# Kernel optimization log

Hardware: AMD Instinct MI355X
Metric: run time of the kernel (lower is better)

## Reference

```python
import jax, jax.numpy as jnp
import numpy as np
import math

N_CELLS = 65536
HIDDEN = 128
IN_DIM = 64
MAX_DEG = 6
BOND_P = 0.5


def _build_graph():
    """2D lattice bond percolation -> padded adjacency [n, MAX_DEG] + signs + mask."""
    rng = np.random.default_rng(0)
    side = int(math.ceil(math.sqrt(N_CELLS)))
    adj = [[] for _ in range(N_CELLS)]
    for i in range(N_CELLS):
        col = i % side
        r = i + 1
        if col + 1 < side and r < N_CELLS and rng.random() < BOND_P:
            adj[i].append(r); adj[r].append(i)
        d = i + side
        if d < N_CELLS and rng.random() < BOND_P:
            adj[i].append(d); adj[d].append(i)
    for i in range(N_CELLS):  # ring fix for isolated nodes
        if not adj[i]:
            r = (i + 1) % N_CELLS
            adj[i].append(r); adj[r].append(i)
    sign_map = {}
    for i in range(N_CELLS):
        for j in adj[i]:
            key = (min(i, j), max(i, j))
            if key not in sign_map:
                sign_map[key] = 1.0 if rng.random() > 0.5 else -1.0
    nbr = np.zeros((N_CELLS, MAX_DEG), np.int32)
    sgn = np.ones((N_CELLS, MAX_DEG), np.float32)
    msk = np.zeros((N_CELLS, MAX_DEG), bool)
    for i in range(N_CELLS):
        for k, j in enumerate(adj[i][:MAX_DEG]):
            nbr[i, k] = j
            msk[i, k] = True
            sgn[i, k] = sign_map[(min(i, j), max(i, j))]
    return nbr, sgn, msk


def setup_inputs() -> dict:
    key = jax.random.key(0)
    ks = jax.random.split(key, 8)
    nbr, sgn, msk = _build_graph()
    n = N_CELLS
    cell_amp = jax.random.uniform(ks[0], (n, HIDDEN)) * 0.5 + 0.5
    cell_phase = jax.random.normal(ks[1], (n, HIDDEN)) * 0.5 \
        + (2.0 * jnp.pi * jnp.arange(n, dtype=jnp.float32) / n)[:, None]
    phase_vel = jax.random.normal(ks[2], (n, HIDDEN)) * 0.05
    return {
        'x': jax.random.normal(ks[3], (1, IN_DIM)),
        'cell_amp': cell_amp.astype(jnp.float32),
        'cell_phase': cell_phase.astype(jnp.float32),
        'phase_vel': phase_vel.astype(jnp.float32),
        'nbr_idx': jnp.asarray(nbr),
        'nbr_sign': jnp.asarray(sgn),
        'nbr_mask': jnp.asarray(msk),
        'W_in': jax.random.normal(ks[4], (HIDDEN, IN_DIM)) * 0.05,
        'b_in': jax.random.normal(ks[5], (HIDDEN,)) * 0.05,
        'W_dec': jax.random.normal(ks[6], (IN_DIM, 2 * HIDDEN)) * 0.05,
        'b_dec': jax.random.normal(ks[7], (IN_DIM,)) * 0.05,
        'step': 1,
    }


def reference(x, cell_amp, cell_phase, phase_vel, nbr_idx, nbr_sign, nbr_mask,
              W_in, b_in, W_dec, b_dec, step):
    n, h = cell_amp.shape
    # complex cell states, then phase-velocity rotation
    states = (cell_amp * jnp.exp(1j * cell_phase)).astype(jnp.complex64)
    states = states * jnp.exp(1j * phase_vel * 0.1)
    ang = jnp.angle(states)                               # [n, h]

    # --- neighbor interference (vectorized gather over padded adjacency) ---
    nbr_states = states[nbr_idx]                          # [n, d, h]
    nbr_ang = ang[nbr_idx]                                # [n, d, h]
    coupling = jnp.cos(ang[:, None, :] - nbr_ang) * nbr_sign[:, :, None]
    contrib = jnp.where(nbr_mask[:, :, None], coupling * nbr_states * 0.1, 0.0)
    interference = contrib.sum(axis=1)                    # [n, h]
    deg = nbr_mask.sum(axis=-1)                           # [n]
    new = 0.7 * states + 0.3 * interference / jnp.maximum(deg, 1)[:, None]
    new = jnp.where((deg > 0)[:, None], new, states)      # 'continue' for isolated nodes

    # --- morphism toward strongest neighbor (argmax over neighbors) ---
    strength = jnp.abs(states).sum(axis=-1)               # [n]
    nstr = jnp.where(nbr_mask, strength[nbr_idx], -jnp.inf)
    best_slot = jnp.argmax(nstr, axis=1)                  # first max, like python max()
    best = jnp.take_along_axis(nbr_idx, best_slot[:, None], axis=1)[:, 0]
    src = states[best]                                    # [n, h]
    morph = jnp.abs(src) * jnp.exp(1j * (jnp.angle(new) - jnp.angle(src)))
    new = jnp.where((deg >= 2)[:, None], new + 0.02 * morph, new)

    # --- global traveling wave ---
    t = step * 0.1
    wave = 0.02 * jnp.sin(t + 2.0 * jnp.pi * jnp.arange(n, dtype=jnp.float32) / n)
    new = new * (1.0 + wave)[:, None]

    # --- input-driven phase perturbation on first 32 cells ---
    sig = x[0] @ W_in.T + b_in                            # [h]
    pp = sig / (jnp.abs(sig).max() + 1e-8) * jnp.pi * 0.1
    idx = jnp.arange(n, dtype=jnp.float32)
    factor = jnp.where(jnp.arange(n) < 32, 0.1 / (1.0 + 0.1 * idx), 0.0)
    new_ang = jnp.angle(new) + pp[None, :] * factor[:, None]
    new = jnp.abs(new) * jnp.exp(1j * new_ang)

    # --- amplitude renormalization per cell ---
    amp = jnp.abs(new)
    amp = amp / (amp.max(axis=-1, keepdims=True) + 1e-8)
    cs = (amp * jnp.exp(1j * jnp.angle(new))).astype(jnp.complex64)

    # --- readout ---
    mean_state = cs.mean(axis=0)                          # [h]
    out_real = jnp.concatenate([mean_state.real, mean_state.imag])[None, :]
    pred = out_real @ W_dec.T + b_dec                     # [1, IN_DIM]
    tension = jnp.var(jnp.abs(cs), ddof=1)                # torch.var (unbiased)
    return pred, tension
```

## Files before the change

### kernel.cpp

```cpp
#include <hip/hip_runtime.h>
#include <hip/hip_fp16.h>
#include <math.h>

#define N_CELLS 65536
#define HIDDEN  128
#define IN_DIM  64
#define MAX_DEG 6

#define WPB    4
#define NPB    32
#define NBLK   (N_CELLS/NPB)
#define CHUNK  4
#define NXCD   8

#define INV2PI 0.15915494309189535f

typedef _Float16 h2f __attribute__((ext_vector_type(2)));

__device__ __forceinline__ void fsincos(float x, float& s, float& c) {
    const float r = x * INV2PI;
    s = __builtin_amdgcn_sinf(r);
    c = __builtin_amdgcn_cosf(r);
}

#define WS_PP    0
#define WS_FLAG  512
#define WS_STR   1024
#define WS_S     (1024 + N_CELLS*4)
#define WS_ADJ   (WS_S + (size_t)N_CELLS*512)
#define WS_P     (WS_ADJ + (size_t)N_CELLS*32)
#define WS_SA    (WS_P + 256*NBLK*4)
#define WS_SA2   (WS_SA + NBLK*4)
#define WS_MEAN  (WS_SA2 + NBLK*4)

__global__ __launch_bounds__(256) void k_pre(
    const float* __restrict__ amp, const float* __restrict__ phase,
    const float* __restrict__ vel,
    const float* __restrict__ x, const float* __restrict__ W_in,
    const float* __restrict__ b_in, const unsigned char* __restrict__ maskb,
    int4* __restrict__ S, float* __restrict__ strength,
    float* __restrict__ pp, int* __restrict__ flag)
{
    const int tid = threadIdx.x;
    const int bx  = blockIdx.x;
    if (bx < N_CELLS/8) {
        const int blkp = (bx & (NXCD-1)) * (N_CELLS/8/NXCD) + (bx >> 3);
        const int node = blkp*8 + (tid >> 5);
        const int hl   = tid & 31;
        const size_t ro = (size_t)node*HIDDEN + 4*hl;
        const float4 a = *(const float4*)(amp   + ro);
        const float4 p = *(const float4*)(phase + ro);
        const float4 v = *(const float4*)(vel   + ro);
        float s0,c0,s1,c1,s2,c2,s3,c3;
        fsincos(fmaf(0.1f, v.x, p.x), s0, c0);
        fsincos(fmaf(0.1f, v.y, p.y), s1, c1);
        fsincos(fmaf(0.1f, v.z, p.z), s2, c2);
        fsincos(fmaf(0.1f, v.w, p.w), s3, c3);
        union { int4 v4; __half2 h[4]; } u;
        u.h[0] = __floats2half2_rn(a.x*c0, a.x*s0);
        u.h[1] = __floats2half2_rn(a.y*c1, a.y*s1);
        u.h[2] = __floats2half2_rn(a.z*c2, a.z*s2);
        u.h[3] = __floats2half2_rn(a.w*c3, a.w*s3);
        S[(size_t)node*32 + hl] = u.v4;
        float st = a.x + a.y + a.z + a.w;
        #pragma unroll
        for (int off = 16; off > 0; off >>= 1) st += __shfl_xor(st, off);
        if (hl == 0) strength[node] = st;
        return;
    }
    __shared__ float sig[HIDDEN];
    __shared__ float red[HIDDEN];
    __shared__ int fl[256];
    if (tid < HIDDEN) {
        float acc = b_in[tid];
        #pragma unroll 8
        for (int d = 0; d < IN_DIM; ++d) acc = fmaf(W_in[tid*IN_DIM + d], x[d], acc);
        sig[tid] = acc;
        red[tid] = fabsf(acc);
    }
    int v = 0;
    #pragma unroll
    for (int r = 0; r < 4; ++r) v |= (int)maskb[(tid + 256*r)*4 + 1];
    fl[tid] = v;
    __syncthreads();
    for (int s = 64; s > 0; s >>= 1) {
        if (tid < s) red[tid] = fmaxf(red[tid], red[tid + s]);
        __syncthreads();
    }
    for (int s = 128; s > 0; s >>= 1) {
        if (tid < s) fl[tid] |= fl[tid + s];
        __syncthreads();
    }
    if (tid < HIDDEN) pp[tid] = sig[tid] / (red[0] + 1e-8f) * 0.314159265358979f;
    if (tid == 0) *flag = (fl[0] != 0) ? 1 : 0;
}

__global__ __launch_bounds__(256) void k_adj(
    const int* __restrict__ nbr_idx, const float* __restrict__ nbr_sign,
    const void* __restrict__ nbr_mask, const int* __restrict__ flagp,
    const float* __restrict__ strength, int4* __restrict__ adj)
{
    __shared__ int   lw[256][MAX_DEG];
    __shared__ float ls[256][MAX_DEG];
    const int t = threadIdx.x;
    const int bx = blockIdx.x;
    const int blkp = (bx & (NXCD-1)) * (N_CELLS/256/NXCD) + (bx >> 3);
    const int i = blkp*256 + t;
    const int flagv = *flagp;
    const unsigned char* mb = (const unsigned char*)nbr_mask;
    const int*           mi = (const int*)nbr_mask;
    int cnt = 0;
    #pragma unroll
    for (int k = 0; k < MAX_DEG; ++k) {
        const int e = i*MAX_DEG + k;
        const int m = flagv ? (mb[e] != 0) : (mi[e] != 0);
        const int j = nbr_idx[e];
        const float sg = nbr_sign[e];
        if (m) {
            lw[t][cnt] = j | ((sg < 0.0f) ? (1<<24) : 0) | (1<<25);
            ls[t][cnt] = strength[j];
            ++cnt;
        }
    }
    #pragma unroll
    for (int k = 0; k < MAX_DEG; ++k) if (k >= cnt) lw[t][k] = 0;
    int cb = 0; float bv = ls[t][0];
    #pragma unroll
    for (int k = 1; k < MAX_DEG; ++k)
        if (k < cnt && ls[t][k] > bv) { bv = ls[t][k]; cb = k; }
    adj[2*(size_t)i    ] = make_int4(lw[t][0], lw[t][1], lw[t][2], lw[t][3]);
    adj[2*(size_t)i + 1] = make_int4(lw[t][4], lw[t][5], cnt | (cb << 8), 0);
}

__global__ __launch_bounds__(256) void k_mainc(
    const int4* __restrict__ S, const int4* __restrict__ adj,
    const int* __restrict__ step, const float* __restrict__ pp,
    float* __restrict__ P, float* __restrict__ p_sa, float* __restrict__ p_sa2)
{
    __shared__ float4 lredre[WPB][32], lredim[WPB][32];
    __shared__ float  lsa[WPB], lsa2[WPB];

    const int tid   = threadIdx.x;
    const int bx    = blockIdx.x;
    const int blk   = (bx & (NXCD-1)) * (NBLK/NXCD) + (bx >> 3);
    const int node0 = blk * NPB;

    const int wv   = tid >> 6;
    const int lane = tid & 63;
    const int half = lane >> 5;
    const int lh   = lane & 31;
    const float trev = 0.1f * (float)step[0] * INV2PI;
    const float4 ppv = ((const float4*)pp)[lh];

    float accre[4] = {0,0,0,0}, accim[4] = {0,0,0,0};
    float accsa = 0.f, accsa2 = 0.f;

    const int nlbase = wv*(2*CHUNK) + half;
    int4 A0n = adj[2*(size_t)(node0 + nlbase)    ];
    int4 A1n = adj[2*(size_t)(node0 + nlbase) + 1];

    #pragma unroll 1
    for (int c = 0; c < CHUNK; ++c) {
        const int nl = nlbase + 2*c;
        const int i  = node0 + nl;
        const int4 A0 = A0n, A1 = A1n;
        if (c + 1 < CHUNK) {
            A0n = adj[2*(size_t)(i + 2)    ];
            A1n = adj[2*(size_t)(i + 2) + 1];
        }
        const int deg = A1.z & 0xFF;
        const int cb  = A1.z >> 8;
        const int slots[MAX_DEG] = {A0.x, A0.y, A0.z, A0.w, A1.x, A1.y};

        union H { int4 v4; h2f h[4]; int w[4]; };
        H us, nb[MAX_DEG];
        us.v4 = S[(size_t)(unsigned)i*32 + lh];
        #pragma unroll
        for (int k = 0; k < MAX_DEG; ++k)
            if (k < deg) nb[k].v4 = S[(size_t)(unsigned)(slots[k] & 0xFFFF)*32 + lh];

        float R[4], I[4], inva[4];
        #pragma unroll
        for (int q = 0; q < 4; ++q) {
            R[q] = (float)us.h[q].x;
            I[q] = (float)us.h[q].y;
            inva[q] = __builtin_amdgcn_rsqf(
                __builtin_amdgcn_fdot2(us.h[q], us.h[q], 0.0f, false));
        }

        float ir[4] = {0,0,0,0}, ii[4] = {0,0,0,0};
        #pragma unroll
        for (int k = 0; k < MAX_DEG; ++k) {
            if (k < deg) {
                const int w = slots[k];
                const float sgnm = (w & (1<<24)) ? -1.0f : 1.0f;
                #pragma unroll
                for (int q = 0; q < 4; ++q) {
                    const float E   = __builtin_amdgcn_fdot2(us.h[q], nb[k].h[q], 0.0f, false);
                    const float aj2 = __builtin_amdgcn_fdot2(nb[k].h[q], nb[k].h[q], 0.0f, false);
                    const float g = sgnm * E * __builtin_amdgcn_rsqf(aj2);
                    ir[q] = fmaf(g, (float)nb[k].h[q].x, ir[q]);
                    ii[q] = fmaf(g, (float)nb[k].h[q].y, ii[q]);
                }
            }
        }

        H ub;
        #pragma unroll
        for (int q = 0; q < 4; ++q) {
            int v = nb[0].w[q];
            #pragma unroll
            for (int k = 1; k < MAX_DEG; ++k)
                if (k < deg) v = (k == cb) ? nb[k].w[q] : v;
            ub.w[q] = v;
        }

        const float f = 0.03f * __builtin_amdgcn_rcpf((float)deg);
        float nr[4], ni[4];
        #pragma unroll
        for (int q = 0; q < 4; ++q) {
            const float fq = f * inva[q];
            nr[q] = fmaf(0.7f, R[q], fq*ir[q]);
            ni[q] = fmaf(0.7f, I[q], fq*ii[q]);
        }

        if (deg >= 2) {
            #pragma unroll
            for (int q = 0; q < 4; ++q) {
                const float ex = (float)ub.h[q].x, ey = (float)ub.h[q].y;
                const float im = 0.02f * __builtin_amdgcn_rsqf(nr[q]*nr[q] + ni[q]*ni[q]);
                const float mr = im*(nr[q]*ex + ni[q]*ey);
                const float mi = im*(ni[q]*ex - nr[q]*ey);
                nr[q] += mr; ni[q] += mi;
            }
        }

        const float wr = fmaf((float)i, 1.52587890625e-5f, trev);
        const float wf = 1.0f + 0.02f * __builtin_amdgcn_sinf(wr);
        #pragma unroll
        for (int q = 0; q < 4; ++q) { nr[q] *= wf; ni[q] *= wf; }

        if (i < 32) {
            const float fac = 0.1f / fmaf(0.1f, (float)i, 1.0f);
            const float pv[4] = {ppv.x, ppv.y, ppv.z, ppv.w};
            #pragma unroll
            for (int q = 0; q < 4; ++q) {
                float sp, cp;
                fsincos(pv[q]*fac, sp, cp);
                const float tr = nr[q]*cp - ni[q]*sp;
                ni[q] = ni[q]*cp + nr[q]*sp;
                nr[q] = tr;
            }
        }

        float m[4];
        #pragma unroll
        for (int q = 0; q < 4; ++q) m[q] = sqrtf(nr[q]*nr[q] + ni[q]*ni[q]);
        float lm = fmaxf(fmaxf(m[0], m[1]), fmaxf(m[2], m[3]));
        #pragma unroll
        for (int off = 16; off > 0; off >>= 1) lm = fmaxf(lm, __shfl_xor(lm, off));
        const float sc = 1.0f / (lm + 1e-8f);
        #pragma unroll
        for (int q = 0; q < 4; ++q) {
            accre[q] += nr[q]*sc;
            accim[q] += ni[q]*sc;
            const float A = m[q]*sc;
            accsa  += A;
            accsa2 += A*A;
        }
    }

    #pragma unroll
    for (int q = 0; q < 4; ++q) {
        accre[q] += __shfl_xor(accre[q], 32);
        accim[q] += __shfl_xor(accim[q], 32);
    }
    #pragma unroll
    for (int off = 32; off > 0; off >>= 1) {
        accsa  += __shfl_xor(accsa,  off);
        accsa2 += __shfl_xor(accsa2, off);
    }
    if (half == 0) {
        lredre[wv][lh] = make_float4(accre[0], accre[1], accre[2], accre[3]);
        lredim[wv][lh] = make_float4(accim[0], accim[1], accim[2], accim[3]);
    }
    if (lane == 0) { lsa[wv] = accsa; lsa2[wv] = accsa2; }
    __syncthreads();
    if (tid < 32) {
        float4 r = lredre[0][tid], im = lredim[0][tid];
        #pragma unroll
        for (int w = 1; w < WPB; ++w) {
            const float4 a = lredre[w][tid], b = lredim[w][tid];
            r.x += a.x; r.y += a.y; r.z += a.z; r.w += a.w;
            im.x += b.x; im.y += b.y; im.z += b.z; im.w += b.w;
        }
        P[(4*tid  )*NBLK + blk]       = r.x;
        P[(4*tid+1)*NBLK + blk]       = r.y;
        P[(4*tid+2)*NBLK + blk]       = r.z;
        P[(4*tid+3)*NBLK + blk]       = r.w;
        P[(128+4*tid  )*NBLK + blk]   = im.x;
        P[(128+4*tid+1)*NBLK + blk]   = im.y;
        P[(128+4*tid+2)*NBLK + blk]   = im.z;
        P[(128+4*tid+3)*NBLK + blk]   = im.w;
    }
    if (tid == 0) {
        p_sa [blk] = lsa[0]  + lsa[1]  + lsa[2]  + lsa[3];
        p_sa2[blk] = lsa2[0] + lsa2[1] + lsa2[2] + lsa2[3];
    }
}

__global__ void k_red(const float* __restrict__ P, float* __restrict__ mean)
{
    __shared__ double red[256];
    const int r = blockIdx.x, tid = threadIdx.x;
    double s = 0.0;
    #pragma unroll
    for (int k = 0; k < NBLK/256; ++k) s += (double)P[(size_t)r*NBLK + tid + 256*k];
    red[tid] = s;
    __syncthreads();
    for (int st = 128; st > 0; st >>= 1) { if (tid < st) red[tid] += red[tid + st]; __syncthreads(); }
    if (tid == 0) mean[r] = (float)(red[0] / (double)N_CELLS);
}

__global__ void k_final(const float* __restrict__ mean_in,
                        const float* __restrict__ p_sa, const float* __restrict__ p_sa2,
                        const float* __restrict__ W_dec, const float* __restrict__ b_dec,
                        float* __restrict__ out)
{
    __shared__ float  mean[2*HIDDEN];
    __shared__ double dred[256];
    __shared__ double tots[2];
    const int tid = threadIdx.x;
    mean[tid] = mean_in[tid];
    double sa = 0.0, sa2 = 0.0;
    #pragma unroll
    for (int k = 0; k < NBLK/256; ++k) {
        sa  += (double)p_sa [tid + 256*k];
        sa2 += (double)p_sa2[tid + 256*k];
    }
    dred[tid] = sa;
    __syncthreads();
    for (int s = 128; s > 0; s >>= 1) { if (tid < s) dred[tid] += dred[tid + s]; __syncthreads(); }
    if (tid == 0) tots[0] = dred[0];
    __syncthreads();
    dred[tid] = sa2;
    __syncthreads();
    for (int s = 128; s > 0; s >>= 1) { if (tid < s) dred[tid] += dred[tid + s]; __syncthreads(); }
    if (tid == 0) tots[1] = dred[0];
    __syncthreads();

    if (tid < IN_DIM) {
        float acc = b_dec[tid];
        #pragma unroll 8
        for (int c = 0; c < 2*HIDDEN; ++c) acc = fmaf(mean[c], W_dec[tid*2*HIDDEN + c], acc);
        out[tid] = acc;
    }
    if (tid == 0) {
        const double M = (double)N_CELLS * (double)HIDDEN;
        const double var = (tots[1] - tots[0]*tots[0]/M) / (M - 1.0);
        out[IN_DIM] = (float)var;
    }
}

extern "C" void kernel_launch(void* const* d_in, const int* in_sizes, int n_in,
                              void* d_out, int out_size, void* d_ws, size_t ws_size,
                              hipStream_t stream)
{
    const float* x       = (const float*)d_in[0];
    const float* amp     = (const float*)d_in[1];
    const float* phase   = (const float*)d_in[2];
    const float* vel     = (const float*)d_in[3];
    const int*   nbr_idx = (const int*)d_in[4];
    const float* nbr_sgn = (const float*)d_in[5];
    const void*  nbr_msk = d_in[6];
    const float* W_in    = (const float*)d_in[7];
    const float* b_in    = (const float*)d_in[8];
    const float* W_dec   = (const float*)d_in[9];
    const float* b_dec   = (const float*)d_in[10];
    const int*   step    = (const int*)d_in[11];

    char* wsb = (char*)d_ws;
    float* pp    = (float*)(wsb + WS_PP);
    int*   flag  = (int*)  (wsb + WS_FLAG);
    float* strg  = (float*)(wsb + WS_STR);
    int4*  S     = (int4*) (wsb + WS_S);
    int4*  adjv  = (int4*) (wsb + WS_ADJ);
    float* P     = (float*)(wsb + WS_P);
    float* p_sa  = (float*)(wsb + WS_SA);
    float* p_sa2 = (float*)(wsb + WS_SA2);
    float* meanb = (float*)(wsb + WS_MEAN);
    float* out   = (float*)d_out;

    k_pre<<<N_CELLS/8 + 1, 256, 0, stream>>>(amp, phase, vel, x, W_in, b_in,
                                             (const unsigned char*)nbr_msk,
                                             S, strg, pp, flag);
    k_adj<<<N_CELLS/256, 256, 0, stream>>>(nbr_idx, nbr_sgn, nbr_msk, flag, strg, adjv);
    k_mainc<<<NBLK, 256, 0, stream>>>(S, adjv, step, pp, P, p_sa, p_sa2);
    k_red<<<256, 256, 0, stream>>>(P, meanb);
    k_final<<<1, 256, 0, stream>>>(meanb, p_sa, p_sa2, W_dec, b_dec, out);
}
```

Before: 67.27 us.

## Precompute best neighbor in slot 0 and make per-wave gather loop uniform

The adjacency build kernel now swaps the strongest-coupled neighbor into slot 0 and pads empty slots with the node itself. It also stores the max degree of each node pair, and the two half-waves of a wave process such a pair. The main kernel loops to that wave-uniform bound, using a validity bit to zero the padded contributions. This drops the per-lane divergent branches, the cb select over the neighbors, and the divergent deg>=2 branch. The cost is extra gathers of padded self entries, plus a shared-memory sync in the adjacency kernel.

```diff
diff --git a/kernel.cpp b/kernel.cpp
--- a/kernel.cpp
+++ b/kernel.cpp
@@ -102,6 +102,7 @@
 {
     __shared__ int   lw[256][MAX_DEG];
     __shared__ float ls[256][MAX_DEG];
+    __shared__ int   ldeg[256];
     const int t = threadIdx.x;
     const int bx = blockIdx.x;
     const int blkp = (bx & (NXCD-1)) * (N_CELLS/256/NXCD) + (bx >> 3);
@@ -122,14 +123,22 @@
             ++cnt;
         }
     }
-    #pragma unroll
-    for (int k = 0; k < MAX_DEG; ++k) if (k >= cnt) lw[t][k] = 0;
     int cb = 0; float bv = ls[t][0];
     #pragma unroll
     for (int k = 1; k < MAX_DEG; ++k)
         if (k < cnt && ls[t][k] > bv) { bv = ls[t][k]; cb = k; }
+    if (cb != 0) {
+        const int tmp = lw[t][0];
+        lw[t][0] = lw[t][cb];
+        lw[t][cb] = tmp;
+    }
+    #pragma unroll
+    for (int k = 0; k < MAX_DEG; ++k) if (k >= cnt) lw[t][k] = i;
+    ldeg[t] = cnt;
+    __syncthreads();
+    const int kmax = max(cnt, ldeg[t ^ 1]);
     adj[2*(size_t)i    ] = make_int4(lw[t][0], lw[t][1], lw[t][2], lw[t][3]);
-    adj[2*(size_t)i + 1] = make_int4(lw[t][4], lw[t][5], cnt | (cb << 8), 0);
+    adj[2*(size_t)i + 1] = make_int4(lw[t][4], lw[t][5], cnt, kmax);
 }
 
 __global__ __launch_bounds__(256) void k_mainc(
@@ -168,8 +177,8 @@
             A0n = adj[2*(size_t)(i + 2)    ];
             A1n = adj[2*(size_t)(i + 2) + 1];
         }
-        const int deg = A1.z & 0xFF;
-        const int cb  = A1.z >> 8;
+        const int deg  = A1.z;
+        const int kmax = __builtin_amdgcn_readfirstlane(A1.w);
         const int slots[MAX_DEG] = {A0.x, A0.y, A0.z, A0.w, A1.x, A1.y};
 
         union H { int4 v4; h2f h[4]; int w[4]; };
@@ -177,7 +186,7 @@
         us.v4 = S[(size_t)(unsigned)i*32 + lh];
         #pragma unroll
         for (int k = 0; k < MAX_DEG; ++k)
-            if (k < deg) nb[k].v4 = S[(size_t)(unsigned)(slots[k] & 0xFFFF)*32 + lh];
+            if (k < kmax) nb[k].v4 = S[(size_t)(unsigned)(slots[k] & 0xFFFF)*32 + lh];
 
         float R[4], I[4], inva[4];
         #pragma unroll
@@ -191,9 +200,10 @@
         float ir[4] = {0,0,0,0}, ii[4] = {0,0,0,0};
         #pragma unroll
         for (int k = 0; k < MAX_DEG; ++k) {
-            if (k < deg) {
+            if (k < kmax) {
                 const int w = slots[k];
-                const float sgnm = (w & (1<<24)) ? -1.0f : 1.0f;
+                const float vf = (float)((w >> 25) & 1);
+                const float sgnm = (w & (1<<24)) ? -vf : vf;
                 #pragma unroll
                 for (int q = 0; q < 4; ++q) {
                     const float E   = __builtin_amdgcn_fdot2(us.h[q], nb[k].h[q], 0.0f, false);
@@ -205,16 +215,6 @@
             }
         }
 
-        H ub;
-        #pragma unroll
-        for (int q = 0; q < 4; ++q) {
-            int v = nb[0].w[q];
-            #pragma unroll
-            for (int k = 1; k < MAX_DEG; ++k)
-                if (k < deg) v = (k == cb) ? nb[k].w[q] : v;
-            ub.w[q] = v;
-        }
-
         const float f = 0.03f * __builtin_amdgcn_rcpf((float)deg);
         float nr[4], ni[4];
         #pragma unroll
@@ -224,15 +224,15 @@
             ni[q] = fmaf(0.7f, I[q], fq*ii[q]);
         }
 
-        if (deg >= 2) {
-            #pragma unroll
-            for (int q = 0; q < 4; ++q) {
-                const float ex = (float)ub.h[q].x, ey = (float)ub.h[q].y;
-                const float im = 0.02f * __builtin_amdgcn_rsqf(nr[q]*nr[q] + ni[q]*ni[q]);
-                const float mr = im*(nr[q]*ex + ni[q]*ey);
-                const float mi = im*(ni[q]*ex - nr[q]*ey);
-                nr[q] += mr; ni[q] += mi;
-            }
+        const float g2 = (deg >= 2) ? 0.02f : 0.0f;
+        #pragma unroll
+        for (int q = 0; q < 4; ++q) {
+            const float ex = (float)nb[0].h[q].x, ey = (float)nb[0].h[q].y;
+            const float im = g2 * __builtin_amdgcn_rsqf(
+                fmaxf(nr[q]*nr[q] + ni[q]*ni[q], 1e-30f));
+            const float mr = im*(nr[q]*ex + ni[q]*ey);
+            const float mi = im*(ni[q]*ex - nr[q]*ey);
+            nr[q] += mr; ni[q] += mi;
         }
 
         const float wr = fmaf((float)i, 1.52587890625e-5f, trev);
```

Result: no change. 66.43 us (-1.3%).
